# Optimization experiments

Measured on AMD Instinct MI355X. Metric: run time of the kernel, lower is better.

## Reference

```python
import jax, jax.numpy as jnp
import numpy as np

H, HKV, D, HID, I, S = 32, 8, 128, 4096, 12288, 8192
EPS = 1e-6


def _rms(x, w):
    # RMSNorm over last dim (ANERMSNorm)
    return x * jax.lax.rsqrt(jnp.mean(x * x, axis=-1, keepdims=True) + EPS) * w


def _rotate_half(x):
    x1, x2 = jnp.split(x, 2, axis=-1)
    return jnp.concatenate([-x2, x1], axis=-1)


def setup_inputs() -> dict:
    key = jax.random.key(0)
    ks = jax.random.split(key, 12)
    std = 0.02
    pos = 1000.0
    # RoPE angles for this position (HF convention: emb = concat(freqs, freqs))
    inv_freq = 1.0 / (10000.0 ** (np.arange(0, D, 2, dtype=np.float32) / D))
    ang = np.concatenate([pos * inv_freq, pos * inv_freq])  # (D,)
    return {
        "hidden_conv": jax.random.normal(ks[0], (1, HID, 1, 1), jnp.float32),
        "position": jnp.array([pos], jnp.float32),
        "cos": jnp.asarray(np.cos(ang), jnp.float32).reshape(1, 1, D),
        "sin": jnp.asarray(np.sin(ang), jnp.float32).reshape(1, 1, D),
        "k_cache": jax.random.normal(ks[1], (1, HKV, S, D), jnp.float32),
        "v_cache": jax.random.normal(ks[2], (1, HKV, S, D), jnp.float32),
        "Wq": jax.random.normal(ks[3], (H * D, HID), jnp.float32) * std,
        "Wk": jax.random.normal(ks[4], (HKV * D, HID), jnp.float32) * std,
        "Wv": jax.random.normal(ks[5], (HKV * D, HID), jnp.float32) * std,
        "Wo": jax.random.normal(ks[6], (HID, H * D), jnp.float32) * std,
        "Wg": jax.random.normal(ks[7], (I, HID), jnp.float32) * std,
        "Wu": jax.random.normal(ks[8], (I, HID), jnp.float32) * std,
        "Wd": jax.random.normal(ks[9], (HID, I), jnp.float32) * std,
        "q_norm_w": jnp.ones((D,), jnp.float32),
        "k_norm_w": jnp.ones((D,), jnp.float32),
        "ln1_w": jnp.ones((HID,), jnp.float32),
        "ln2_w": jnp.ones((HID,), jnp.float32),
    }


def reference(hidden_conv, position, cos, sin, k_cache, v_cache,
              Wq, Wk, Wv, Wo, Wg, Wu, Wd,
              q_norm_w, k_norm_w, ln1_w, ln2_w):
    x = hidden_conv.reshape(HID)                      # conv layout -> vector
    residual = x
    h = _rms(x, ln1_w)
    # 1x1 conv projections == GEMV
    q = (Wq @ h).reshape(H, D)
    k = (Wk @ h).reshape(HKV, D)
    v = (Wv @ h).reshape(HKV, D)
    q = _rms(q, q_norm_w)
    k = _rms(k, k_norm_w)
    c, s = cos.reshape(D), sin.reshape(D)
    q = q * c + _rotate_half(q) * s
    k = k * c + _rotate_half(k) * s
    # mask-based KV cache write (scatter-free, as in original)
    pos = position.reshape(())
    positions = jnp.arange(S, dtype=jnp.float32)
    wmask = (positions == pos)[None, :, None]          # (1, S, 1)
    k_new = jnp.where(wmask, k[:, None, :], k_cache[0])  # (HKV, S, D)
    v_new = jnp.where(wmask, v[:, None, :], v_cache[0])
    # GQA repeat
    rep = H // HKV
    k_rep = jnp.repeat(k_new, rep, axis=0)             # (H, S, D)
    v_rep = jnp.repeat(v_new, rep, axis=0)
    scale = D ** -0.5
    scores = jnp.einsum('hd,hsd->hs', q, k_rep) * scale
    causal = jnp.where(positions > pos, jnp.float32(-10000.0), jnp.float32(0.0))
    attn = jax.nn.softmax(scores + causal, axis=-1)
    out = jnp.einsum('hs,hsd->hd', attn, v_rep).reshape(H * D)
    h1 = residual + Wo @ out
    # SwiGLU MLP
    h2 = _rms(h1, ln2_w)
    mlp = Wd @ (jax.nn.silu(Wg @ h2) * (Wu @ h2))
    hid = h1 + mlp
    return (hid.reshape(1, HID, 1, 1), k_new[None], v_new[None])
```

## Files before the change

kernel.cpp:

```cpp
#include <hip/hip_runtime.h>
#include <cstdint>
#include <cmath>

#define H 32
#define HKV 8
#define DD 128
#define HID 4096
#define II 12288
#define SS 8192
#define EPSF 1e-6f
#define CS 256
#define NC (SS / CS)

__device__ __forceinline__ float wave_reduce_sum(float v) {
#pragma unroll
    for (int off = 32; off; off >>= 1) v += __shfl_down(v, off, 64);
    return v;
}

__global__ __launch_bounds__(256) void rms_kernel(const float* __restrict__ x,
                                                  const float* __restrict__ w,
                                                  float* __restrict__ out, int n) {
    __shared__ float red[4];
    int t = threadIdx.x;
    int lane = t & 63, wave = t >> 6;
    const float4* x4 = (const float4*)x;
    int n4 = n >> 2;
    float ss = 0.f;
    for (int i = t; i < n4; i += 256) {
        float4 a = x4[i];
        ss += a.x * a.x + a.y * a.y + a.z * a.z + a.w * a.w;
    }
    ss = wave_reduce_sum(ss);
    if (lane == 0) red[wave] = ss;
    __syncthreads();
    float tot = red[0] + red[1] + red[2] + red[3];
    float r = rsqrtf(tot / (float)n + EPSF);
    const float4* w4 = (const float4*)w;
    float4* o4 = (float4*)out;
    for (int i = t; i < n4; i += 256) {
        float4 a = x4[i], b = w4[i];
        o4[i] = make_float4(a.x * r * b.x, a.y * r * b.y, a.z * r * b.z, a.w * r * b.w);
    }
}

__global__ __launch_bounds__(256) void gemv_qkv(const float* __restrict__ Wq,
                                                const float* __restrict__ Wk,
                                                const float* __restrict__ Wv,
                                                const float* __restrict__ h,
                                                float* __restrict__ q,
                                                float* __restrict__ k,
                                                float* __restrict__ v) {
    int wave = threadIdx.x >> 6, lane = threadIdx.x & 63;
    int row = blockIdx.x * 4 + wave;
    const float* wrow;
    float* out;
    int r;
    if (row < 4096) { wrow = Wq + (size_t)row * HID; out = q; r = row; }
    else if (row < 5120) { wrow = Wk + (size_t)(row - 4096) * HID; out = k; r = row - 4096; }
    else { wrow = Wv + (size_t)(row - 5120) * HID; out = v; r = row - 5120; }
    const float4* w4 = (const float4*)wrow;
    const float4* h4 = (const float4*)h;
    float acc = 0.f;
#pragma unroll
    for (int ii = 0; ii < 16; ii++) {
        int i = lane + ii * 64;
        float4 a = w4[i], b = h4[i];
        acc += a.x * b.x + a.y * b.y + a.z * b.z + a.w * b.w;
    }
    acc = wave_reduce_sum(acc);
    if (lane == 0) out[r] = acc;
}

__global__ __launch_bounds__(128) void qk_norm_rope(float* __restrict__ q,
                                                    float* __restrict__ k,
                                                    const float* __restrict__ cv,
                                                    const float* __restrict__ sv,
                                                    const float* __restrict__ qw,
                                                    const float* __restrict__ kw) {
    int b = blockIdx.x, t = threadIdx.x;
    bool isq = (b < H);
    float* vec = isq ? (q + (size_t)b * DD) : (k + (size_t)(b - H) * DD);
    const float* nw = isq ? qw : kw;
    __shared__ float sh[DD];
    __shared__ float red[DD];
    float val = vec[t];
    red[t] = val * val;
    __syncthreads();
#pragma unroll
    for (int off = 64; off; off >>= 1) {
        if (t < off) red[t] += red[t + off];
        __syncthreads();
    }
    float r = rsqrtf(red[0] / (float)DD + EPSF);
    float nv = val * r * nw[t];
    sh[t] = nv;
    __syncthreads();
    float other = (t < 64) ? -sh[t + 64] : sh[t - 64];
    vec[t] = nv * cv[t] + other * sv[t];
}

__global__ __launch_bounds__(256) void kv_copy(const float* __restrict__ kc,
                                               const float* __restrict__ vc,
                                               const float* __restrict__ kn,
                                               const float* __restrict__ vn,
                                               const float* __restrict__ position,
                                               float* __restrict__ ok,
                                               float* __restrict__ ov) {
    int pos = (int)position[0];
    size_t i = (size_t)blockIdx.x * 256 + threadIdx.x;
    const float4* src4 = (blockIdx.y == 0) ? (const float4*)kc : (const float4*)vc;
    const float4* new4 = (blockIdx.y == 0) ? (const float4*)kn : (const float4*)vn;
    float4* dst4 = (blockIdx.y == 0) ? (float4*)ok : (float4*)ov;
    int s = (int)((i >> 5) & (SS - 1));
    float4 val;
    if (s == pos) {
        int head = (int)(i >> 18);
        int d4 = (int)(i & 31);
        val = new4[head * 32 + d4];
    } else {
        val = src4[i];
    }
    dst4[i] = val;
}

__global__ __launch_bounds__(256) void attn_partial(const float* __restrict__ q,
                                                    const float* __restrict__ ok,
                                                    const float* __restrict__ ov,
                                                    const float* __restrict__ position,
                                                    float* __restrict__ pm,
                                                    float* __restrict__ pl,
                                                    float* __restrict__ po) {
    int h = blockIdx.x, c = blockIdx.y, t = threadIdx.x;
    int kvh = h >> 2;
    int pos = (int)position[0];
    __shared__ float qs[DD];
    __shared__ float red[CS];
    __shared__ float pv[CS];
    if (t < DD) qs[t] = q[h * DD + t];
    __syncthreads();
    int s = c * CS + t;
    float score = -INFINITY;
    if (s <= pos) {
        const float4* kr = (const float4*)(ok + ((size_t)kvh * SS + s) * DD);
        const float4* q4 = (const float4*)qs;
        float acc = 0.f;
#pragma unroll
        for (int i = 0; i < DD / 4; i++) {
            float4 a = kr[i], b = q4[i];
            acc += a.x * b.x + a.y * b.y + a.z * b.z + a.w * b.w;
        }
        score = acc * 0.08838834764831845f;
    }
    red[t] = score;
    __syncthreads();
#pragma unroll
    for (int off = 128; off; off >>= 1) {
        if (t < off) red[t] = fmaxf(red[t], red[t + off]);
        __syncthreads();
    }
    float m = red[0];
    __syncthreads();
    float p = (score == -INFINITY) ? 0.f : expf(score - m);
    pv[t] = p;
    red[t] = p;
    __syncthreads();
#pragma unroll
    for (int off = 128; off; off >>= 1) {
        if (t < off) red[t] += red[t + off];
        __syncthreads();
    }
    float l = red[0];
    int jend = pos + 1 - c * CS;
    if (jend > CS) jend = CS;
    if (t < DD) {
        float acc = 0.f;
        for (int j = 0; j < jend; j++) {
            acc += pv[j] * ov[((size_t)kvh * SS + (size_t)(c * CS + j)) * DD + t];
        }
        po[((size_t)h * NC + c) * DD + t] = acc;
    }
    if (t == 0) {
        pm[h * NC + c] = m;
        pl[h * NC + c] = l;
    }
}

__global__ __launch_bounds__(128) void attn_combine(const float* __restrict__ pm,
                                                    const float* __restrict__ pl,
                                                    const float* __restrict__ po,
                                                    float* __restrict__ ao) {
    int h = blockIdx.x, d = threadIdx.x;
    float M = -INFINITY;
    for (int c = 0; c < NC; c++) M = fmaxf(M, pm[h * NC + c]);
    float L = 0.f, acc = 0.f;
    for (int c = 0; c < NC; c++) {
        float mm = pm[h * NC + c];
        if (mm == -INFINITY) continue;
        float wgt = expf(mm - M);
        L += wgt * pl[h * NC + c];
        acc += wgt * po[((size_t)h * NC + c) * DD + d];
    }
    ao[h * DD + d] = acc / L;
}

__global__ __launch_bounds__(256) void gemv_wo(const float* __restrict__ W,
                                               const float* __restrict__ xin,
                                               const float* __restrict__ resid,
                                               float* __restrict__ out) {
    int wave = threadIdx.x >> 6, lane = threadIdx.x & 63;
    int row = blockIdx.x * 4 + wave;
    const float4* w4 = (const float4*)(W + (size_t)row * HID);
    const float4* x4 = (const float4*)xin;
    float acc = 0.f;
#pragma unroll
    for (int ii = 0; ii < 16; ii++) {
        int i = lane + ii * 64;
        float4 a = w4[i], b = x4[i];
        acc += a.x * b.x + a.y * b.y + a.z * b.z + a.w * b.w;
    }
    acc = wave_reduce_sum(acc);
    if (lane == 0) out[row] = resid[row] + acc;
}

__global__ __launch_bounds__(256) void gemv_gateup(const float* __restrict__ Wg,
                                                   const float* __restrict__ Wu,
                                                   const float* __restrict__ h2,
                                                   float* __restrict__ m) {
    int wave = threadIdx.x >> 6, lane = threadIdx.x & 63;
    int row = blockIdx.x * 4 + wave;
    const float4* g4 = (const float4*)(Wg + (size_t)row * HID);
    const float4* u4 = (const float4*)(Wu + (size_t)row * HID);
    const float4* x4 = (const float4*)h2;
    float accg = 0.f, accu = 0.f;
#pragma unroll
    for (int ii = 0; ii < 16; ii++) {
        int i = lane + ii * 64;
        float4 b = x4[i];
        float4 a = g4[i];
        accg += a.x * b.x + a.y * b.y + a.z * b.z + a.w * b.w;
        float4 cvu = u4[i];
        accu += cvu.x * b.x + cvu.y * b.y + cvu.z * b.z + cvu.w * b.w;
    }
    accg = wave_reduce_sum(accg);
    accu = wave_reduce_sum(accu);
    if (lane == 0) {
        float g = accg;
        m[row] = (g / (1.f + expf(-g))) * accu;
    }
}

__global__ __launch_bounds__(256) void gemv_down(const float* __restrict__ Wd,
                                                 const float* __restrict__ mi,
                                                 const float* __restrict__ h1,
                                                 float* __restrict__ out) {
    int wave = threadIdx.x >> 6, lane = threadIdx.x & 63;
    int row = blockIdx.x * 4 + wave;
    const float4* w4 = (const float4*)(Wd + (size_t)row * II);
    const float4* x4 = (const float4*)mi;
    float acc = 0.f;
#pragma unroll
    for (int ii = 0; ii < 48; ii++) {
        int i = lane + ii * 64;
        float4 a = w4[i], b = x4[i];
        acc += a.x * b.x + a.y * b.y + a.z * b.z + a.w * b.w;
    }
    acc = wave_reduce_sum(acc);
    if (lane == 0) out[row] = h1[row] + acc;
}

extern "C" void kernel_launch(void* const* d_in, const int* in_sizes, int n_in,
                              void* d_out, int out_size, void* d_ws, size_t ws_size,
                              hipStream_t stream) {
    const float* x        = (const float*)d_in[0];
    const float* position = (const float*)d_in[1];
    const float* cosv     = (const float*)d_in[2];
    const float* sinv     = (const float*)d_in[3];
    const float* k_cache  = (const float*)d_in[4];
    const float* v_cache  = (const float*)d_in[5];
    const float* Wq       = (const float*)d_in[6];
    const float* Wk       = (const float*)d_in[7];
    const float* Wv       = (const float*)d_in[8];
    const float* Wo       = (const float*)d_in[9];
    const float* Wg       = (const float*)d_in[10];
    const float* Wu       = (const float*)d_in[11];
    const float* Wd       = (const float*)d_in[12];
    const float* q_norm_w = (const float*)d_in[13];
    const float* k_norm_w = (const float*)d_in[14];
    const float* ln1_w    = (const float*)d_in[15];
    const float* ln2_w    = (const float*)d_in[16];

    float* out_hid = (float*)d_out;
    float* out_k   = out_hid + HID;
    float* out_v   = out_k + (size_t)HKV * SS * DD;

    float* ws = (float*)d_ws;
    float* h        = ws;
    float* q        = h + HID;
    float* k        = q + H * DD;
    float* v        = k + HKV * DD;
    float* attn_out = v + HKV * DD;
    float* h1       = attn_out + H * DD;
    float* h2       = h1 + HID;
    float* mi       = h2 + HID;
    float* part_m   = mi + II;
    float* part_l   = part_m + H * NC;
    float* part_o   = part_l + H * NC;

    rms_kernel<<<1, 256, 0, stream>>>(x, ln1_w, h, HID);
    gemv_qkv<<<1536, 256, 0, stream>>>(Wq, Wk, Wv, h, q, k, v);
    qk_norm_rope<<<H + HKV, 128, 0, stream>>>(q, k, cosv, sinv, q_norm_w, k_norm_w);
    kv_copy<<<dim3(8192, 2), 256, 0, stream>>>(k_cache, v_cache, k, v, position, out_k, out_v);
    attn_partial<<<dim3(H, NC), 256, 0, stream>>>(q, out_k, out_v, position, part_m, part_l, part_o);
    attn_combine<<<H, 128, 0, stream>>>(part_m, part_l, part_o, attn_out);
    gemv_wo<<<1024, 256, 0, stream>>>(Wo, attn_out, x, h1);
    rms_kernel<<<1, 256, 0, stream>>>(h1, ln2_w, h2, HID);
    gemv_gateup<<<3072, 256, 0, stream>>>(Wg, Wu, h2, mi);
    gemv_down<<<1024, 256, 0, stream>>>(Wd, mi, h1, out_hid);
}
```

Before: 711.0 us.

## Fuse RMSNorms into GEMVs, split KV copy, use nontemporal weight loads

The standalone single-block RMSNorm kernels are folded into the QKV and gate/up GEMVs: each block recomputes the sum of squares and scales the dot product afterwards. The KV cache copy becomes a plain bulk nontemporal copy with no position check, and the new K/V row is written by the rope kernel afterwards. Attention chunks past the current position exit early. Weight streams use nontemporal loads. This trades two serial launches and the per-element position test for redundant per-block norm work and an ordering dependency between the bulk copy and the row insert.

New measurement: 695.8 us. -2.1%, faster.

```diff
diff --git a/kernel.cpp b/kernel.cpp
--- a/kernel.cpp
+++ b/kernel.cpp
@@ -12,75 +12,96 @@
 #define CS 256
 #define NC (SS / CS)
 
+typedef float f4 __attribute__((ext_vector_type(4)));
+
 __device__ __forceinline__ float wave_reduce_sum(float v) {
 #pragma unroll
     for (int off = 32; off; off >>= 1) v += __shfl_down(v, off, 64);
     return v;
 }
 
-__global__ __launch_bounds__(256) void rms_kernel(const float* __restrict__ x,
-                                                  const float* __restrict__ w,
-                                                  float* __restrict__ out, int n) {
-    __shared__ float red[4];
-    int t = threadIdx.x;
-    int lane = t & 63, wave = t >> 6;
-    const float4* x4 = (const float4*)x;
-    int n4 = n >> 2;
-    float ss = 0.f;
-    for (int i = t; i < n4; i += 256) {
-        float4 a = x4[i];
-        ss += a.x * a.x + a.y * a.y + a.z * a.z + a.w * a.w;
-    }
-    ss = wave_reduce_sum(ss);
-    if (lane == 0) red[wave] = ss;
-    __syncthreads();
-    float tot = red[0] + red[1] + red[2] + red[3];
-    float r = rsqrtf(tot / (float)n + EPSF);
-    const float4* w4 = (const float4*)w;
-    float4* o4 = (float4*)out;
-    for (int i = t; i < n4; i += 256) {
-        float4 a = x4[i], b = w4[i];
-        o4[i] = make_float4(a.x * r * b.x, a.y * r * b.y, a.z * r * b.z, a.w * r * b.w);
+__device__ __forceinline__ f4 ntload(const f4* p) {
+    return __builtin_nontemporal_load(p);
+}
+
+__global__ __launch_bounds__(256) void kv_bulk(const float* __restrict__ kc,
+                                               const float* __restrict__ vc,
+                                               float* __restrict__ ok,
+                                               float* __restrict__ ov) {
+    const f4* src = (blockIdx.y == 0) ? (const f4*)kc : (const f4*)vc;
+    f4* dst = (blockIdx.y == 0) ? (f4*)ok : (f4*)ov;
+    size_t base = (size_t)blockIdx.x * 1024 + threadIdx.x;
+#pragma unroll
+    for (int j = 0; j < 4; j++) {
+        size_t i = base + (size_t)j * 256;
+        __builtin_nontemporal_store(ntload(src + i), dst + i);
     }
 }
 
 __global__ __launch_bounds__(256) void gemv_qkv(const float* __restrict__ Wq,
                                                 const float* __restrict__ Wk,
                                                 const float* __restrict__ Wv,
-                                                const float* __restrict__ h,
+                                                const float* __restrict__ x,
+                                                const float* __restrict__ ln1,
                                                 float* __restrict__ q,
                                                 float* __restrict__ k,
                                                 float* __restrict__ v) {
-    int wave = threadIdx.x >> 6, lane = threadIdx.x & 63;
+    __shared__ float red[4];
+    int t = threadIdx.x;
+    int wave = t >> 6, lane = t & 63;
+    const f4* x4 = (const f4*)x;
+    const f4* l4 = (const f4*)ln1;
+    float ss = 0.f;
+#pragma unroll
+    for (int i = 0; i < 4; i++) {
+        f4 a = x4[t + i * 256];
+        ss += a.x * a.x + a.y * a.y + a.z * a.z + a.w * a.w;
+    }
+    ss = wave_reduce_sum(ss);
+    if (lane == 0) red[wave] = ss;
+    __syncthreads();
+    float r = rsqrtf((red[0] + red[1] + red[2] + red[3]) * (1.f / (float)HID) + EPSF);
+
     int row = blockIdx.x * 4 + wave;
     const float* wrow;
     float* out;
-    int r;
-    if (row < 4096) { wrow = Wq + (size_t)row * HID; out = q; r = row; }
-    else if (row < 5120) { wrow = Wk + (size_t)(row - 4096) * HID; out = k; r = row - 4096; }
-    else { wrow = Wv + (size_t)(row - 5120) * HID; out = v; r = row - 5120; }
-    const float4* w4 = (const float4*)wrow;
-    const float4* h4 = (const float4*)h;
+    int ro;
+    if (row < 4096)      { wrow = Wq + (size_t)row * HID;          out = q; ro = row; }
+    else if (row < 5120) { wrow = Wk + (size_t)(row - 4096) * HID; out = k; ro = row - 4096; }
+    else                 { wrow = Wv + (size_t)(row - 5120) * HID; out = v; ro = row - 5120; }
+    const f4* w4 = (const f4*)wrow;
     float acc = 0.f;
 #pragma unroll
     for (int ii = 0; ii < 16; ii++) {
         int i = lane + ii * 64;
-        float4 a = w4[i], b = h4[i];
-        acc += a.x * b.x + a.y * b.y + a.z * b.z + a.w * b.w;
+        f4 a = ntload(w4 + i);
+        f4 b = x4[i];
+        f4 c = l4[i];
+        acc += a.x * b.x * c.x + a.y * b.y * c.y + a.z * b.z * c.z + a.w * b.w * c.w;
     }
     acc = wave_reduce_sum(acc);
-    if (lane == 0) out[r] = acc;
-}
-
-__global__ __launch_bounds__(128) void qk_norm_rope(float* __restrict__ q,
-                                                    float* __restrict__ k,
-                                                    const float* __restrict__ cv,
-                                                    const float* __restrict__ sv,
-                                                    const float* __restrict__ qw,
-                                                    const float* __restrict__ kw) {
+    if (lane == 0) out[ro] = acc * r;
+}
+
+__global__ __launch_bounds__(128) void rope_insert(float* __restrict__ q,
+                                                   const float* __restrict__ k,
+                                                   const float* __restrict__ v,
+                                                   const float* __restrict__ cv,
+                                                   const float* __restrict__ sv,
+                                                   const float* __restrict__ qw,
+                                                   const float* __restrict__ kw,
+                                                   const float* __restrict__ position,
+                                                   float* __restrict__ ok,
+                                                   float* __restrict__ ov) {
     int b = blockIdx.x, t = threadIdx.x;
+    int pos = (int)position[0];
+    if (b >= 40) {
+        int hv = b - 40;
+        ov[((size_t)hv * SS + pos) * DD + t] = v[hv * DD + t];
+        return;
+    }
     bool isq = (b < H);
-    float* vec = isq ? (q + (size_t)b * DD) : (k + (size_t)(b - H) * DD);
+    const float* vec = isq ? (q + (size_t)b * DD) : (k + (size_t)(b - H) * DD);
     const float* nw = isq ? qw : kw;
     __shared__ float sh[DD];
     __shared__ float red[DD];
@@ -92,36 +113,18 @@
         if (t < off) red[t] += red[t + off];
         __syncthreads();
     }
-    float r = rsqrtf(red[0] / (float)DD + EPSF);
+    float r = rsqrtf(red[0] * (1.f / (float)DD) + EPSF);
     float nv = val * r * nw[t];
     sh[t] = nv;
     __syncthreads();
     float other = (t < 64) ? -sh[t + 64] : sh[t - 64];
-    vec[t] = nv * cv[t] + other * sv[t];
-}
-
-__global__ __launch_bounds__(256) void kv_copy(const float* __restrict__ kc,
-                                               const float* __restrict__ vc,
-                                               const float* __restrict__ kn,
-                                               const float* __restrict__ vn,
-                                               const float* __restrict__ position,
-                                               float* __restrict__ ok,
-                                               float* __restrict__ ov) {
-    int pos = (int)position[0];
-    size_t i = (size_t)blockIdx.x * 256 + threadIdx.x;
-    const float4* src4 = (blockIdx.y == 0) ? (const float4*)kc : (const float4*)vc;
-    const float4* new4 = (blockIdx.y == 0) ? (const float4*)kn : (const float4*)vn;
-    float4* dst4 = (blockIdx.y == 0) ? (float4*)ok : (float4*)ov;
-    int s = (int)((i >> 5) & (SS - 1));
-    float4 val;
-    if (s == pos) {
-        int head = (int)(i >> 18);
-        int d4 = (int)(i & 31);
-        val = new4[head * 32 + d4];
+    float res = nv * cv[t] + other * sv[t];
+    if (isq) {
+        q[(size_t)b * DD + t] = res;
     } else {
-        val = src4[i];
-    }
-    dst4[i] = val;
+        int hk = b - H;
+        ok[((size_t)hk * SS + pos) * DD + t] = res;
+    }
 }
 
 __global__ __launch_bounds__(256) void attn_partial(const float* __restrict__ q,
@@ -134,6 +137,10 @@
     int h = blockIdx.x, c = blockIdx.y, t = threadIdx.x;
     int kvh = h >> 2;
     int pos = (int)position[0];
+    if (c * CS > pos) {
+        if (t == 0) { pm[h * NC + c] = -INFINITY; pl[h * NC + c] = 0.f; }
+        return;
+    }
     __shared__ float qs[DD];
     __shared__ float red[CS];
     __shared__ float pv[CS];
@@ -142,12 +149,12 @@
     int s = c * CS + t;
     float score = -INFINITY;
     if (s <= pos) {
-        const float4* kr = (const float4*)(ok + ((size_t)kvh * SS + s) * DD);
-        const float4* q4 = (const float4*)qs;
+        const f4* kr = (const f4*)(ok + ((size_t)kvh * SS + s) * DD);
+        const f4* q4 = (const f4*)qs;
         float acc = 0.f;
 #pragma unroll
         for (int i = 0; i < DD / 4; i++) {
-            float4 a = kr[i], b = q4[i];
+            f4 a = kr[i], b = q4[i];
             acc += a.x * b.x + a.y * b.y + a.z * b.z + a.w * b.w;
         }
         score = acc * 0.08838834764831845f;
@@ -210,13 +217,14 @@
                                                float* __restrict__ out) {
     int wave = threadIdx.x >> 6, lane = threadIdx.x & 63;
     int row = blockIdx.x * 4 + wave;
-    const float4* w4 = (const float4*)(W + (size_t)row * HID);
-    const float4* x4 = (const float4*)xin;
+    const f4* w4 = (const f4*)(W + (size_t)row * HID);
+    const f4* x4 = (const f4*)xin;
     float acc = 0.f;
 #pragma unroll
     for (int ii = 0; ii < 16; ii++) {
         int i = lane + ii * 64;
-        float4 a = w4[i], b = x4[i];
+        f4 a = ntload(w4 + i);
+        f4 b = x4[i];
         acc += a.x * b.x + a.y * b.y + a.z * b.z + a.w * b.w;
     }
     acc = wave_reduce_sum(acc);
@@ -225,28 +233,45 @@
 
 __global__ __launch_bounds__(256) void gemv_gateup(const float* __restrict__ Wg,
                                                    const float* __restrict__ Wu,
-                                                   const float* __restrict__ h2,
+                                                   const float* __restrict__ h1,
+                                                   const float* __restrict__ ln2,
                                                    float* __restrict__ m) {
-    int wave = threadIdx.x >> 6, lane = threadIdx.x & 63;
+    __shared__ float red[4];
+    int t = threadIdx.x;
+    int wave = t >> 6, lane = t & 63;
+    const f4* x4 = (const f4*)h1;
+    const f4* l4 = (const f4*)ln2;
+    float ss = 0.f;
+#pragma unroll
+    for (int i = 0; i < 4; i++) {
+        f4 a = x4[t + i * 256];
+        ss += a.x * a.x + a.y * a.y + a.z * a.z + a.w * a.w;
+    }
+    ss = wave_reduce_sum(ss);
+    if (lane == 0) red[wave] = ss;
+    __syncthreads();
+    float r = rsqrtf((red[0] + red[1] + red[2] + red[3]) * (1.f / (float)HID) + EPSF);
+
     int row = blockIdx.x * 4 + wave;
-    const float4* g4 = (const float4*)(Wg + (size_t)row * HID);
-    const float4* u4 = (const float4*)(Wu + (size_t)row * HID);
-    const float4* x4 = (const float4*)h2;
+    const f4* g4 = (const f4*)(Wg + (size_t)row * HID);
+    const f4* u4 = (const f4*)(Wu + (size_t)row * HID);
     float accg = 0.f, accu = 0.f;
 #pragma unroll
     for (int ii = 0; ii < 16; ii++) {
         int i = lane + ii * 64;
-        float4 b = x4[i];
-        float4 a = g4[i];
-        accg += a.x * b.x + a.y * b.y + a.z * b.z + a.w * b.w;
-        float4 cvu = u4[i];
-        accu += cvu.x * b.x + cvu.y * b.y + cvu.z * b.z + cvu.w * b.w;
+        f4 b = x4[i];
+        f4 c = l4[i];
+        f4 hb; hb.x = b.x * c.x; hb.y = b.y * c.y; hb.z = b.z * c.z; hb.w = b.w * c.w;
+        f4 a = ntload(g4 + i);
+        accg += a.x * hb.x + a.y * hb.y + a.z * hb.z + a.w * hb.w;
+        f4 u = ntload(u4 + i);
+        accu += u.x * hb.x + u.y * hb.y + u.z * hb.z + u.w * hb.w;
     }
     accg = wave_reduce_sum(accg);
     accu = wave_reduce_sum(accu);
     if (lane == 0) {
-        float g = accg;
-        m[row] = (g / (1.f + expf(-g))) * accu;
+        float g = accg * r, uu = accu * r;
+        m[row] = (g / (1.f + expf(-g))) * uu;
     }
 }
 
@@ -256,14 +281,17 @@
                                                  float* __restrict__ out) {
     int wave = threadIdx.x >> 6, lane = threadIdx.x & 63;
     int row = blockIdx.x * 4 + wave;
-    const float4* w4 = (const float4*)(Wd + (size_t)row * II);
-    const float4* x4 = (const float4*)mi;
+    const f4* w4 = (const f4*)(Wd + (size_t)row * II);
+    const f4* x4 = (const f4*)mi;
     float acc = 0.f;
-#pragma unroll
-    for (int ii = 0; ii < 48; ii++) {
-        int i = lane + ii * 64;
-        float4 a = w4[i], b = x4[i];
-        acc += a.x * b.x + a.y * b.y + a.z * b.z + a.w * b.w;
+    for (int o = 0; o < 3; o++) {
+#pragma unroll
+        for (int ii = 0; ii < 16; ii++) {
+            int i = lane + (o * 16 + ii) * 64;
+            f4 a = ntload(w4 + i);
+            f4 b = x4[i];
+            acc += a.x * b.x + a.y * b.y + a.z * b.z + a.w * b.w;
+        }
     }
     acc = wave_reduce_sum(acc);
     if (lane == 0) out[row] = h1[row] + acc;
@@ -295,26 +323,24 @@
     float* out_v   = out_k + (size_t)HKV * SS * DD;
 
     float* ws = (float*)d_ws;
-    float* h        = ws;
-    float* q        = h + HID;
+    float* q        = ws;
     float* k        = q + H * DD;
     float* v        = k + HKV * DD;
     float* attn_out = v + HKV * DD;
     float* h1       = attn_out + H * DD;
-    float* h2       = h1 + HID;
-    float* mi       = h2 + HID;
+    float* mi       = h1 + HID;
     float* part_m   = mi + II;
     float* part_l   = part_m + H * NC;
     float* part_o   = part_l + H * NC;
 
-    rms_kernel<<<1, 256, 0, stream>>>(x, ln1_w, h, HID);
-    gemv_qkv<<<1536, 256, 0, stream>>>(Wq, Wk, Wv, h, q, k, v);
-    qk_norm_rope<<<H + HKV, 128, 0, stream>>>(q, k, cosv, sinv, q_norm_w, k_norm_w);
-    kv_copy<<<dim3(8192, 2), 256, 0, stream>>>(k_cache, v_cache, k, v, position, out_k, out_v);
-    attn_partial<<<dim3(H, NC), 256, 0, stream>>>(q, out_k, out_v, position, part_m, part_l, part_o);
+    kv_bulk<<<dim3(2048, 2), 256, 0, stream>>>(k_cache, v_cache, out_k, out_v);
+    gemv_qkv<<<1536, 256, 0, stream>>>(Wq, Wk, Wv, x, ln1_w, q, k, v);
+    rope_insert<<<48, 128, 0, stream>>>(q, k, v, cosv, sinv, q_norm_w, k_norm_w,
+                                        position, out_k, out_v);
+    attn_partial<<<dim3(H, NC), 256, 0, stream>>>(q, out_k, out_v, position,
+                                                  part_m, part_l, part_o);
     attn_combine<<<H, 128, 0, stream>>>(part_m, part_l, part_o, attn_out);
     gemv_wo<<<1024, 256, 0, stream>>>(Wo, attn_out, x, h1);
-    rms_kernel<<<1, 256, 0, stream>>>(h1, ln2_w, h2, HID);
-    gemv_gateup<<<3072, 256, 0, stream>>>(Wg, Wu, h2, mi);
+    gemv_gateup<<<3072, 256, 0, stream>>>(Wg, Wu, h1, ln2_w, mi);
     gemv_down<<<1024, 256, 0, stream>>>(Wd, mi, h1, out_hid);
 }
```
